# Kernel optimization log

Measured on AMD Instinct MI355X. Metric: run time of the kernel, lower is better.

## Reference

```python
import jax, jax.numpy as jnp
import numpy as np

INPUT_SIZE = 1024
HIDDEN_SIZE = 1024
BATCH = 4096


def setup_inputs() -> dict:
    key = jax.random.key(0)
    ks = jax.random.split(key, 16)
    s_in = 1.0 / np.sqrt(INPUT_SIZE)
    s_h = 1.0 / np.sqrt(HIDDEN_SIZE)
    inp = {
        "incoming": jax.random.normal(ks[0], (BATCH, INPUT_SIZE), jnp.float32),
        "old_h": jax.random.normal(ks[1], (BATCH, HIDDEN_SIZE), jnp.float32),
        "old_c": jax.random.normal(ks[2], (BATCH, HIDDEN_SIZE), jnp.float32),
    }
    # torch nn.Linear weights: [out, in]; y = x @ W.T + b
    names = ["i", "o", "f", "c"]
    for j, n in enumerate(names):
        inp[f"w_{n}"] = jax.random.normal(ks[3 + 3 * j], (HIDDEN_SIZE, INPUT_SIZE), jnp.float32) * s_in
        inp[f"b_{n}"] = jax.random.normal(ks[4 + 3 * j], (HIDDEN_SIZE,), jnp.float32) * s_in
        inp[f"u_{n}"] = jax.random.normal(ks[5 + 3 * j], (HIDDEN_SIZE, HIDDEN_SIZE), jnp.float32) * s_h
    return inp


def reference(incoming, old_h, old_c, w_i, b_i, u_i, w_o, b_o, u_o, w_f, b_f, u_f, w_c, b_c, u_c):
    # Concatenate the 4 input->gate and 4 hidden->gate matrices into two
    # fused GEMMs (same math as the 8 separate Linear calls).
    W = jnp.concatenate([w_i, w_o, w_f, w_c], axis=0)   # [4H, I]
    U = jnp.concatenate([u_i, u_o, u_f, u_c], axis=0)   # [4H, H]
    b = jnp.concatenate([b_i, b_o, b_f, b_c], axis=0)   # [4H]
    gates = incoming @ W.T + old_h @ U.T + b            # [B, 4H]
    gi, go, gf, gc = jnp.split(gates, 4, axis=-1)
    i = jax.nn.sigmoid(gi)
    o = jax.nn.sigmoid(go)
    f = jax.nn.sigmoid(gf)
    c_tilde = jnp.tanh(gc)
    new_c = f * old_c + i * c_tilde
    new_h = o * jnp.tanh(new_c)
    return (new_h, new_c)
```

## Files before the change

### kernel.cpp

```cpp
#include <hip/hip_runtime.h>

typedef __bf16 bf16x8 __attribute__((ext_vector_type(8)));
typedef float f32x4 __attribute__((ext_vector_type(4)));

#define B_  4096
#define IN_ 1024
#define H_  1024
#define KD  2048
#define ND  4096

__device__ __forceinline__ unsigned short f2bf(float f) {
    union { float f; unsigned u; } v; v.f = f;
    unsigned r = v.u + 0x7FFFu + ((v.u >> 16) & 1u);
    return (unsigned short)(r >> 16);
}

__global__ __launch_bounds__(256) void pack_all(const float* __restrict__ x,
                                                const float* __restrict__ h,
                                                const float* __restrict__ wi, const float* __restrict__ ui,
                                                const float* __restrict__ wo, const float* __restrict__ uo,
                                                const float* __restrict__ wf, const float* __restrict__ uf,
                                                const float* __restrict__ wc, const float* __restrict__ uc,
                                                unsigned short* __restrict__ Z,
                                                unsigned short* __restrict__ V) {
    const int bid = blockIdx.x;
    const float* src;
    unsigned short* dst;
    if (bid < 8192) {
        int idx = (bid * 256 + threadIdx.x) * 4;
        int m = idx >> 11;
        int k = idx & (KD - 1);
        src = (k < IN_) ? (x + (size_t)m * IN_ + k)
                        : (h + (size_t)m * H_ + (k - IN_));
        dst = Z + idx;
    } else {
        int idx = ((bid - 8192) * 256 + threadIdx.x) * 4;
        int n = idx >> 11;
        int k = idx & (KD - 1);
        int g = n & 3;
        int r = n >> 2;
        const float* wg = (g == 0) ? wi : (g == 1) ? wo : (g == 2) ? wf : wc;
        const float* ug = (g == 0) ? ui : (g == 1) ? uo : (g == 2) ? uf : uc;
        src = (k < IN_) ? (wg + (size_t)r * IN_ + k)
                        : (ug + (size_t)r * H_ + (k - IN_));
        dst = V + idx;
    }
    float4 v = *(const float4*)src;
    ushort4 o;
    o.x = f2bf(v.x); o.y = f2bf(v.y); o.z = f2bf(v.z); o.w = f2bf(v.w);
    *(ushort4*)dst = o;
}

__global__ __launch_bounds__(256, 4) void gemm_lstm(const unsigned short* __restrict__ Z,
                                                    const unsigned short* __restrict__ V,
                                                    const float* __restrict__ oc,
                                                    const float* __restrict__ bi,
                                                    const float* __restrict__ bo,
                                                    const float* __restrict__ bff,
                                                    const float* __restrict__ bc,
                                                    float* __restrict__ nh,
                                                    float* __restrict__ nc) {
    __shared__ float smem[8192];
    unsigned short* lA = (unsigned short*)smem;
    unsigned short* lB = (unsigned short*)(smem + 4096);

    const int tid  = threadIdx.x;
    const int lane = tid & 63;
    const int w    = tid >> 6;
    const int wr   = w >> 1;
    const int wc   = w & 1;

    const int bid = blockIdx.x;
    const int xcd = bid & 7;
    const int j   = bid >> 3;
    const int bx  = (xcd & 3) * 8 + (j & 7);
    const int by  = (xcd >> 2) * 16 + (j >> 3);
    const int m0  = by * 128;
    const int n0  = bx * 128;

    f32x4 acc[4][4];
#pragma unroll
    for (int i = 0; i < 4; ++i)
#pragma unroll
        for (int jj = 0; jj < 4; ++jj) acc[i][jj] = (f32x4){0.f, 0.f, 0.f, 0.f};

    const int lr = lane >> 3;
    const int lc = ((lane & 7) ^ lr) * 8;
    const unsigned short* gA = Z + (size_t)(m0 + w * 32 + lr) * KD + lc;
    const unsigned short* gB = V + (size_t)(n0 + w * 32 + lr) * KD + lc;
    unsigned short* lAw = lA + w * 32 * 64;
    unsigned short* lBw = lB + w * 32 * 64;

    const int lm = lane & 15;

    for (int k0 = 0; k0 < KD; k0 += 64) {
#pragma unroll
        for (int c = 0; c < 4; ++c) {
            __builtin_amdgcn_global_load_lds(
                (const __attribute__((address_space(1))) void*)(gA + (size_t)c * 8 * KD + k0),
                (__attribute__((address_space(3))) void*)(lAw + c * 512), 16, 0, 0);
            __builtin_amdgcn_global_load_lds(
                (const __attribute__((address_space(1))) void*)(gB + (size_t)c * 8 * KD + k0),
                (__attribute__((address_space(3))) void*)(lBw + c * 512), 16, 0, 0);
        }
        __syncthreads();
#pragma unroll
        for (int ks = 0; ks < 2; ++ks) {
            bf16x8 af[4], bf[4];
            const int cb = ks * 4 + (lane >> 4);
            const int sw = (cb ^ (lm & 7)) * 8;
#pragma unroll
            for (int i = 0; i < 4; ++i) {
                af[i] = *(const bf16x8*)(lA + (wr * 64 + i * 16 + lm) * 64 + sw);
                bf[i] = *(const bf16x8*)(lB + (wc * 64 + i * 16 + lm) * 64 + sw);
            }
#pragma unroll
            for (int mi = 0; mi < 4; ++mi)
#pragma unroll
                for (int ni = 0; ni < 4; ++ni)
                    acc[mi][ni] = __builtin_amdgcn_mfma_f32_16x16x32_bf16(
                        af[mi], bf[ni], acc[mi][ni], 0, 0, 0);
        }
        __syncthreads();
    }

    const int a  = lane >> 4;
    const int b  = (lane >> 2) & 3;
    const int g  = lane & 3;
    const int rowl0 = wr * 64 + 4 * a + g;
    const int hl0   = wc * 16;
    const int h0g   = bx * 32;

    const int rr = tid >> 3;
    const int cc = tid & 7;

#pragma unroll
    for (int p = 0; p < 4; ++p) {
        const int row = p * 32 + rr;
        float4 v = *(const float4*)(oc + (size_t)(m0 + row) * H_ + h0g + 4 * cc);
        *(float4*)(smem + row * 32 + ((4 * cc) ^ ((row & 7) << 2))) = v;
    }
    __syncthreads();

    float hv[4][4], cv[4][4];
#pragma unroll
    for (int ni = 0; ni < 4; ++ni) {
        const int hl = hl0 + ni * 4 + b;
        const int hg = h0g + hl;
        const float vbi = bi[hg];
        const float vbo = bo[hg];
        const float vbf = bff[hg];
        const float vbc = bc[hg];
#pragma unroll
        for (int mi = 0; mi < 4; ++mi) {
            const int rowl = rowl0 + mi * 16;
            const float ocv = smem[rowl * 32 + (hl ^ ((rowl & 7) << 2))];
            float recv[4];
#pragma unroll
            for (int t = 0; t < 4; ++t) {
                float xg = acc[mi][ni][(g ^ t) & 3];
                recv[t] = __shfl_xor(xg, t, 64);
            }
            float gi = recv[g] + vbi;
            float go = recv[g ^ 1] + vbo;
            float gf = recv[g ^ 2] + vbf;
            float gc = recv[g ^ 3] + vbc;
            float iv = 1.f / (1.f + __expf(-gi));
            float ov = 1.f / (1.f + __expf(-go));
            float fv = 1.f / (1.f + __expf(-gf));
            float ct = 1.f - 2.f / (__expf(2.f * gc) + 1.f);
            float c2 = fv * ocv + iv * ct;
            float th = 1.f - 2.f / (__expf(2.f * c2) + 1.f);
            cv[ni][mi] = c2;
            hv[ni][mi] = ov * th;
        }
    }
    __syncthreads();

#pragma unroll
    for (int ni = 0; ni < 4; ++ni)
#pragma unroll
        for (int mi = 0; mi < 4; ++mi) {
            const int rowl = rowl0 + mi * 16;
            const int hl = hl0 + ni * 4 + b;
            const int s = rowl * 32 + (hl ^ ((rowl & 7) << 2));
            smem[s] = cv[ni][mi];
            smem[4096 + s] = hv[ni][mi];
        }
    __syncthreads();

#pragma unroll
    for (int p = 0; p < 4; ++p) {
        const int row = p * 32 + rr;
        const int s = row * 32 + ((4 * cc) ^ ((row & 7) << 2));
        float4 vcn = *(const float4*)(smem + s);
        float4 vhn = *(const float4*)(smem + 4096 + s);
        const size_t go = (size_t)(m0 + row) * H_ + h0g + 4 * cc;
        *(float4*)(nc + go) = vcn;
        *(float4*)(nh + go) = vhn;
    }
}

extern "C" void kernel_launch(void* const* d_in, const int* in_sizes, int n_in,
                              void* d_out, int out_size, void* d_ws, size_t ws_size,
                              hipStream_t stream) {
    const float* incoming = (const float*)d_in[0];
    const float* old_h    = (const float*)d_in[1];
    const float* old_c    = (const float*)d_in[2];
    const float* w_i = (const float*)d_in[3];
    const float* b_i = (const float*)d_in[4];
    const float* u_i = (const float*)d_in[5];
    const float* w_o = (const float*)d_in[6];
    const float* b_o = (const float*)d_in[7];
    const float* u_o = (const float*)d_in[8];
    const float* w_f = (const float*)d_in[9];
    const float* b_f = (const float*)d_in[10];
    const float* u_f = (const float*)d_in[11];
    const float* w_c = (const float*)d_in[12];
    const float* b_c = (const float*)d_in[13];
    const float* u_c = (const float*)d_in[14];

    unsigned short* Z = (unsigned short*)d_ws;
    unsigned short* V = Z + (size_t)B_ * KD;

    pack_all<<<16384, 256, 0, stream>>>(incoming, old_h,
                                        w_i, u_i, w_o, u_o, w_f, u_f, w_c, u_c,
                                        Z, V);
    gemm_lstm<<<1024, 256, 0, stream>>>(
        Z, V, old_c, b_i, b_o, b_f, b_c,
        (float*)d_out, (float*)d_out + (size_t)B_ * H_);
}
```

Before: 208.0 us.

## Use 256x256 tiles with double-buffered LDS and phased prefetch in LSTM GEMM

Replaces the 128x128 single-buffered GEMM with a 256x256 tile computed by 8 waves. It uses 128KB of dynamic LDS split into two buffers, so the next K-slice loads asynchronously while the current one feeds the MFMAs. The K loop runs in four phases, with s_setprio raised around the MFMA blocks and fine-grained vmcnt waits. This aims to hide global-load latency and raise data reuse per block, at the cost of one block per CU, 256 blocks total, and heavier register pressure.

```diff
diff --git a/kernel.cpp b/kernel.cpp
--- a/kernel.cpp
+++ b/kernel.cpp
@@ -8,6 +8,7 @@
 #define H_  1024
 #define KD  2048
 #define ND  4096
+#define NT  32
 
 __device__ __forceinline__ unsigned short f2bf(float f) {
     union { float f; unsigned u; } v; v.f = f;
@@ -51,7 +52,43 @@
     *(ushort4*)dst = o;
 }
 
-__global__ __launch_bounds__(256, 4) void gemm_lstm(const unsigned short* __restrict__ Z,
+#define AS1 __attribute__((address_space(1)))
+#define AS3 __attribute__((address_space(3)))
+
+#define STG(SRC, DST)                                                        \
+    __builtin_amdgcn_global_load_lds((const AS1 void*)(SRC),                 \
+                                     (AS3 void*)(DST), 16, 0, 0);
+
+#define GPHASE(H, Q, STAGES, VMW)                                            \
+  {                                                                          \
+    bf16x8 afr[4][2], bfr[2][2];                                             \
+    _Pragma("unroll") for (int mi = 0; mi < 4; ++mi)                         \
+      _Pragma("unroll") for (int ks = 0; ks < 2; ++ks)                       \
+        afr[mi][ks] = *(const bf16x8*)(lA +                                  \
+            (wr * 128 + (H) * 64 + mi * 16 + lm) * 64 +                      \
+            (((ks * 4 + l4) ^ lm7) * 8));                                    \
+    _Pragma("unroll") for (int ni = 0; ni < 2; ++ni)                         \
+      _Pragma("unroll") for (int ks = 0; ks < 2; ++ks)                       \
+        bfr[ni][ks] = *(const bf16x8*)(lB +                                  \
+            (wc * 64 + (Q) * 32 + ni * 16 + lm) * 64 +                       \
+            (((ks * 4 + l4) ^ lm7) * 8));                                    \
+    STAGES                                                                   \
+    __builtin_amdgcn_s_barrier();                                            \
+    asm volatile("s_waitcnt lgkmcnt(0)" ::: "memory");                       \
+    __builtin_amdgcn_s_setprio(1);                                           \
+    _Pragma("unroll") for (int mi = 0; mi < 4; ++mi)                         \
+      _Pragma("unroll") for (int ni = 0; ni < 2; ++ni)                       \
+        _Pragma("unroll") for (int ks = 0; ks < 2; ++ks)                     \
+          acc[(H) * 4 + mi][(Q) * 2 + ni] =                                  \
+              __builtin_amdgcn_mfma_f32_16x16x32_bf16(                       \
+                  afr[mi][ks], bfr[ni][ks],                                  \
+                  acc[(H) * 4 + mi][(Q) * 2 + ni], 0, 0, 0);                 \
+    __builtin_amdgcn_s_setprio(0);                                           \
+    VMW                                                                      \
+    __builtin_amdgcn_s_barrier();                                            \
+  }
+
+__global__ __launch_bounds__(512, 2) void gemm_lstm(const unsigned short* __restrict__ Z,
                                                     const unsigned short* __restrict__ V,
                                                     const float* __restrict__ oc,
                                                     const float* __restrict__ bi,
@@ -60,89 +97,105 @@
                                                     const float* __restrict__ bc,
                                                     float* __restrict__ nh,
                                                     float* __restrict__ nc) {
-    __shared__ float smem[8192];
-    unsigned short* lA = (unsigned short*)smem;
-    unsigned short* lB = (unsigned short*)(smem + 4096);
+    extern __shared__ char smem[];
 
     const int tid  = threadIdx.x;
     const int lane = tid & 63;
     const int w    = tid >> 6;
-    const int wr   = w >> 1;
-    const int wc   = w & 1;
+    const int wr   = w >> 2;
+    const int wc   = w & 3;
+    const int lm   = lane & 15;
+    const int l4   = lane >> 4;
+    const int lm7  = lm & 7;
 
     const int bid = blockIdx.x;
     const int xcd = bid & 7;
     const int j   = bid >> 3;
-    const int bx  = (xcd & 3) * 8 + (j & 7);
-    const int by  = (xcd >> 2) * 16 + (j >> 3);
-    const int m0  = by * 128;
-    const int n0  = bx * 128;
-
-    f32x4 acc[4][4];
-#pragma unroll
-    for (int i = 0; i < 4; ++i)
+    const int bx  = (xcd & 3) * 4 + (j & 3);
+    const int by  = (xcd >> 2) * 8 + (j >> 2);
+    const int m0  = by * 256;
+    const int n0  = bx * 256;
+
+    f32x4 acc[8][4];
+#pragma unroll
+    for (int i = 0; i < 8; ++i)
 #pragma unroll
         for (int jj = 0; jj < 4; ++jj) acc[i][jj] = (f32x4){0.f, 0.f, 0.f, 0.f};
 
-    const int lr = lane >> 3;
-    const int lc = ((lane & 7) ^ lr) * 8;
-    const unsigned short* gA = Z + (size_t)(m0 + w * 32 + lr) * KD + lc;
-    const unsigned short* gB = V + (size_t)(n0 + w * 32 + lr) * KD + lc;
-    unsigned short* lAw = lA + w * 32 * 64;
-    unsigned short* lBw = lB + w * 32 * 64;
-
-    const int lm = lane & 15;
-
-    for (int k0 = 0; k0 < KD; k0 += 64) {
-#pragma unroll
-        for (int c = 0; c < 4; ++c) {
-            __builtin_amdgcn_global_load_lds(
-                (const __attribute__((address_space(1))) void*)(gA + (size_t)c * 8 * KD + k0),
-                (__attribute__((address_space(3))) void*)(lAw + c * 512), 16, 0, 0);
-            __builtin_amdgcn_global_load_lds(
-                (const __attribute__((address_space(1))) void*)(gB + (size_t)c * 8 * KD + k0),
-                (__attribute__((address_space(3))) void*)(lBw + c * 512), 16, 0, 0);
-        }
-        __syncthreads();
-#pragma unroll
-        for (int ks = 0; ks < 2; ++ks) {
-            bf16x8 af[4], bf[4];
-            const int cb = ks * 4 + (lane >> 4);
-            const int sw = (cb ^ (lm & 7)) * 8;
-#pragma unroll
-            for (int i = 0; i < 4; ++i) {
-                af[i] = *(const bf16x8*)(lA + (wr * 64 + i * 16 + lm) * 64 + sw);
-                bf[i] = *(const bf16x8*)(lB + (wc * 64 + i * 16 + lm) * 64 + sw);
-            }
-#pragma unroll
-            for (int mi = 0; mi < 4; ++mi)
-#pragma unroll
-                for (int ni = 0; ni < 4; ++ni)
-                    acc[mi][ni] = __builtin_amdgcn_mfma_f32_16x16x32_bf16(
-                        af[mi], bf[ni], acc[mi][ni], 0, 0, 0);
-        }
-        __syncthreads();
-    }
+    const int sr  = tid >> 3;
+    const int scw = ((tid & 7) ^ (sr & 7)) * 8;
+    const unsigned short* gAs = Z + (size_t)(m0 + sr) * KD + scw;
+    const unsigned short* gBs = V + (size_t)(n0 + sr) * KD + scw;
+    const int wv1024 = w * 1024;
+
+    {
+        char* sd0 = smem + wv1024;
+        STG(gBs,          sd0 + 32768)
+        STG(gBs + 131072, sd0 + 40960)
+        STG(gBs + 262144, sd0 + 49152)
+        STG(gBs + 393216, sd0 + 57344)
+        STG(gAs,          sd0)
+        STG(gAs + 262144, sd0 + 16384)
+        STG(gAs + 131072, sd0 + 8192)
+        STG(gAs + 393216, sd0 + 24576)
+    }
+    asm volatile("s_waitcnt vmcnt(2)" ::: "memory");
+    __builtin_amdgcn_s_barrier();
+
+#pragma unroll 1
+    for (int t = 0; t < NT - 1; ++t) {
+        const unsigned short* lA = (const unsigned short*)(smem + (t & 1) * 65536);
+        const unsigned short* lB = lA + 16384;
+        char* sd = smem + (((t & 1) ^ 1) * 65536) + wv1024;
+        const int k1 = (t + 1) * 64;
+
+        GPHASE(0, 0,
+               STG(gBs + k1,          sd + 32768)
+               STG(gBs + 131072 + k1, sd + 40960), )
+        GPHASE(0, 1,
+               STG(gBs + 262144 + k1, sd + 49152)
+               STG(gBs + 393216 + k1, sd + 57344),
+               asm volatile("s_waitcnt vmcnt(4)" ::: "memory");)
+        GPHASE(1, 0,
+               STG(gAs + k1,          sd)
+               STG(gAs + 262144 + k1, sd + 16384), )
+        GPHASE(1, 1,
+               STG(gAs + 131072 + k1, sd + 8192)
+               STG(gAs + 393216 + k1, sd + 24576),
+               asm volatile("s_waitcnt vmcnt(2)" ::: "memory");)
+    }
+
+    {
+        const unsigned short* lA = (const unsigned short*)(smem + 65536);
+        const unsigned short* lB = lA + 16384;
+        GPHASE(0, 0, , )
+        GPHASE(0, 1, , asm volatile("s_waitcnt vmcnt(0)" ::: "memory");)
+        GPHASE(1, 0, , )
+        GPHASE(1, 1, , )
+    }
+    __syncthreads();
+
+    float* scf = (float*)smem;
 
     const int a  = lane >> 4;
     const int b  = (lane >> 2) & 3;
     const int g  = lane & 3;
-    const int rowl0 = wr * 64 + 4 * a + g;
+    const int rowl0 = wr * 128 + 4 * a + g;
     const int hl0   = wc * 16;
-    const int h0g   = bx * 32;
-
-    const int rr = tid >> 3;
-    const int cc = tid & 7;
-
-#pragma unroll
-    for (int p = 0; p < 4; ++p) {
+    const int h0g   = bx * 64;
+
+    const int rr = tid >> 4;
+    const int cc = tid & 15;
+
+#pragma unroll
+    for (int p = 0; p < 8; ++p) {
         const int row = p * 32 + rr;
         float4 v = *(const float4*)(oc + (size_t)(m0 + row) * H_ + h0g + 4 * cc);
-        *(float4*)(smem + row * 32 + ((4 * cc) ^ ((row & 7) << 2))) = v;
-    }
-    __syncthreads();
-
-    float hv[4][4], cv[4][4];
+        *(float4*)(scf + row * 64 + ((4 * cc) ^ ((row & 7) << 2))) = v;
+    }
+    __syncthreads();
+
+    float hv[4][8], cv[4][8];
 #pragma unroll
     for (int ni = 0; ni < 4; ++ni) {
         const int hl = hl0 + ni * 4 + b;
@@ -152,9 +205,9 @@
         const float vbf = bff[hg];
         const float vbc = bc[hg];
 #pragma unroll
-        for (int mi = 0; mi < 4; ++mi) {
+        for (int mi = 0; mi < 8; ++mi) {
             const int rowl = rowl0 + mi * 16;
-            const float ocv = smem[rowl * 32 + (hl ^ ((rowl & 7) << 2))];
+            const float ocv = scf[rowl * 64 + (hl ^ ((rowl & 7) << 2))];
             float recv[4];
 #pragma unroll
             for (int t = 0; t < 4; ++t) {
@@ -180,24 +233,24 @@
 #pragma unroll
     for (int ni = 0; ni < 4; ++ni)
 #pragma unroll
-        for (int mi = 0; mi < 4; ++mi) {
+        for (int mi = 0; mi < 8; ++mi) {
             const int rowl = rowl0 + mi * 16;
             const int hl = hl0 + ni * 4 + b;
-            const int s = rowl * 32 + (hl ^ ((rowl & 7) << 2));
-            smem[s] = cv[ni][mi];
-            smem[4096 + s] = hv[ni][mi];
+            const int s = rowl * 64 + (hl ^ ((rowl & 7) << 2));
+            scf[s] = cv[ni][mi];
+            scf[16384 + s] = hv[ni][mi];
         }
     __syncthreads();
 
 #pragma unroll
-    for (int p = 0; p < 4; ++p) {
+    for (int p = 0; p < 8; ++p) {
         const int row = p * 32 + rr;
-        const int s = row * 32 + ((4 * cc) ^ ((row & 7) << 2));
-        float4 vcn = *(const float4*)(smem + s);
-        float4 vhn = *(const float4*)(smem + 4096 + s);
-        const size_t go = (size_t)(m0 + row) * H_ + h0g + 4 * cc;
-        *(float4*)(nc + go) = vcn;
-        *(float4*)(nh + go) = vhn;
+        const int s = row * 64 + ((4 * cc) ^ ((row & 7) << 2));
+        float4 vcn = *(const float4*)(scf + s);
+        float4 vhn = *(const float4*)(scf + 16384 + s);
+        const size_t go_ = (size_t)(m0 + row) * H_ + h0g + 4 * cc;
+        *(float4*)(nc + go_) = vcn;
+        *(float4*)(nh + go_) = vhn;
     }
 }
 
@@ -223,10 +276,18 @@
     unsigned short* Z = (unsigned short*)d_ws;
     unsigned short* V = Z + (size_t)B_ * KD;
 
+    static int smem_set = 0;
+    if (!smem_set) {
+        (void)hipFuncSetAttribute((const void*)gemm_lstm,
+                                  hipFuncAttributeMaxDynamicSharedMemorySize,
+                                  131072);
+        smem_set = 1;
+    }
+
     pack_all<<<16384, 256, 0, stream>>>(incoming, old_h,
                                         w_i, u_i, w_o, u_o, w_f, u_f, w_c, u_c,
                                         Z, V);
-    gemm_lstm<<<1024, 256, 0, stream>>>(
+    gemm_lstm<<<256, 512, 131072, stream>>>(
         Z, V, old_c, b_i, b_o, b_f, b_c,
         (float*)d_out, (float*)d_out + (size_t)B_ * H_);
 }
```

New measurement: 216.6 us. +4.1%, slower.

## Double-buffer LDS tiles to overlap global loads with MFMA compute

Applied to the files above, without the earlier changes.

Switches the GEMM main loop to a two-stage LDS ping-pong: the next K tile is issued via global_load_lds while MFMAs run on the current tile, with one waitcnt+barrier per iteration instead of two. LDS grows to 64KB dynamic shared memory and launch bounds drop to 2 blocks per CU. This hides global load latency but lowers occupancy, which previously hid latency across more resident blocks.

```diff
diff --git a/kernel.cpp b/kernel.cpp
--- a/kernel.cpp
+++ b/kernel.cpp
@@ -8,6 +8,7 @@
 #define H_  1024
 #define KD  2048
 #define ND  4096
+#define NT  32
 
 __device__ __forceinline__ unsigned short f2bf(float f) {
     union { float f; unsigned u; } v; v.f = f;
@@ -51,7 +52,14 @@
     *(ushort4*)dst = o;
 }
 
-__global__ __launch_bounds__(256, 4) void gemm_lstm(const unsigned short* __restrict__ Z,
+#define AS1 __attribute__((address_space(1)))
+#define AS3 __attribute__((address_space(3)))
+
+#define STG(SRC, DST)                                                        \
+    __builtin_amdgcn_global_load_lds((const AS1 void*)(SRC),                 \
+                                     (AS3 void*)(DST), 16, 0, 0);
+
+__global__ __launch_bounds__(256, 2) void gemm_lstm(const unsigned short* __restrict__ Z,
                                                     const unsigned short* __restrict__ V,
                                                     const float* __restrict__ oc,
                                                     const float* __restrict__ bi,
@@ -60,9 +68,9 @@
                                                     const float* __restrict__ bc,
                                                     float* __restrict__ nh,
                                                     float* __restrict__ nc) {
-    __shared__ float smem[8192];
-    unsigned short* lA = (unsigned short*)smem;
-    unsigned short* lB = (unsigned short*)(smem + 4096);
+    extern __shared__ char smem[];
+    unsigned short* sm16 = (unsigned short*)smem;
+    float* scf = (float*)smem;
 
     const int tid  = threadIdx.x;
     const int lane = tid & 63;
@@ -88,22 +96,32 @@
     const int lc = ((lane & 7) ^ lr) * 8;
     const unsigned short* gA = Z + (size_t)(m0 + w * 32 + lr) * KD + lc;
     const unsigned short* gB = V + (size_t)(n0 + w * 32 + lr) * KD + lc;
-    unsigned short* lAw = lA + w * 32 * 64;
-    unsigned short* lBw = lB + w * 32 * 64;
-
+    const int wOffA = w * 2048;
     const int lm = lane & 15;
 
-    for (int k0 = 0; k0 < KD; k0 += 64) {
-#pragma unroll
-        for (int c = 0; c < 4; ++c) {
-            __builtin_amdgcn_global_load_lds(
-                (const __attribute__((address_space(1))) void*)(gA + (size_t)c * 8 * KD + k0),
-                (__attribute__((address_space(3))) void*)(lAw + c * 512), 16, 0, 0);
-            __builtin_amdgcn_global_load_lds(
-                (const __attribute__((address_space(1))) void*)(gB + (size_t)c * 8 * KD + k0),
-                (__attribute__((address_space(3))) void*)(lBw + c * 512), 16, 0, 0);
-        }
-        __syncthreads();
+#pragma unroll
+    for (int c = 0; c < 4; ++c) {
+        STG(gA + (size_t)c * 8 * KD, sm16 + wOffA + c * 512)
+        STG(gB + (size_t)c * 8 * KD, sm16 + 8192 + wOffA + c * 512)
+    }
+    asm volatile("s_waitcnt vmcnt(0)" ::: "memory");
+    __syncthreads();
+
+#pragma unroll 1
+    for (int t = 0; t < NT; ++t) {
+        const unsigned short* lA = sm16 + (t & 1) * 16384;
+        const unsigned short* lB = lA + 8192;
+
+        if (t < NT - 1) {
+            unsigned short* sd = sm16 + ((t & 1) ^ 1) * 16384 + wOffA;
+            const int k1 = (t + 1) * 64;
+#pragma unroll
+            for (int c = 0; c < 4; ++c) {
+                STG(gA + (size_t)c * 8 * KD + k1, sd + c * 512)
+                STG(gB + (size_t)c * 8 * KD + k1, sd + 8192 + c * 512)
+            }
+        }
+
 #pragma unroll
         for (int ks = 0; ks < 2; ++ks) {
             bf16x8 af[4], bf[4];
@@ -121,6 +139,8 @@
                     acc[mi][ni] = __builtin_amdgcn_mfma_f32_16x16x32_bf16(
                         af[mi], bf[ni], acc[mi][ni], 0, 0, 0);
         }
+
+        asm volatile("s_waitcnt vmcnt(0)" ::: "memory");
         __syncthreads();
     }
 
@@ -138,7 +158,7 @@
     for (int p = 0; p < 4; ++p) {
         const int row = p * 32 + rr;
         float4 v = *(const float4*)(oc + (size_t)(m0 + row) * H_ + h0g + 4 * cc);
-        *(float4*)(smem + row * 32 + ((4 * cc) ^ ((row & 7) << 2))) = v;
+        *(float4*)(scf + row * 32 + ((4 * cc) ^ ((row & 7) << 2))) = v;
     }
     __syncthreads();
 
@@ -154,7 +174,7 @@
 #pragma unroll
         for (int mi = 0; mi < 4; ++mi) {
             const int rowl = rowl0 + mi * 16;
-            const float ocv = smem[rowl * 32 + (hl ^ ((rowl & 7) << 2))];
+            const float ocv = scf[rowl * 32 + (hl ^ ((rowl & 7) << 2))];
             float recv[4];
 #pragma unroll
             for (int t = 0; t < 4; ++t) {
@@ -184,8 +204,8 @@
             const int rowl = rowl0 + mi * 16;
             const int hl = hl0 + ni * 4 + b;
             const int s = rowl * 32 + (hl ^ ((rowl & 7) << 2));
-            smem[s] = cv[ni][mi];
-            smem[4096 + s] = hv[ni][mi];
+            scf[s] = cv[ni][mi];
+            scf[4096 + s] = hv[ni][mi];
         }
     __syncthreads();
 
@@ -193,8 +213,8 @@
     for (int p = 0; p < 4; ++p) {
         const int row = p * 32 + rr;
         const int s = row * 32 + ((4 * cc) ^ ((row & 7) << 2));
-        float4 vcn = *(const float4*)(smem + s);
-        float4 vhn = *(const float4*)(smem + 4096 + s);
+        float4 vcn = *(const float4*)(scf + s);
+        float4 vhn = *(const float4*)(scf + 4096 + s);
         const size_t go = (size_t)(m0 + row) * H_ + h0g + 4 * cc;
         *(float4*)(nc + go) = vcn;
         *(float4*)(nh + go) = vhn;
@@ -223,10 +243,18 @@
     unsigned short* Z = (unsigned short*)d_ws;
     unsigned short* V = Z + (size_t)B_ * KD;
 
+    static int smem_set = 0;
+    if (!smem_set) {
+        (void)hipFuncSetAttribute((const void*)gemm_lstm,
+                                  hipFuncAttributeMaxDynamicSharedMemorySize,
+                                  65536);
+        smem_set = 1;
+    }
+
     pack_all<<<16384, 256, 0, stream>>>(incoming, old_h,
                                         w_i, u_i, w_o, u_o, w_f, u_f, w_c, u_c,
                                         Z, V);
-    gemm_lstm<<<1024, 256, 0, stream>>>(
+    gemm_lstm<<<1024, 256, 65536, stream>>>(
         Z, V, old_c, b_i, b_o, b_f, b_c,
         (float*)d_out, (float*)d_out + (size_t)B_ * H_);
 }
```

Measured after the change: 215.5 us. +3.6%, slower.
